# Optimization experiments

Measured on AMD Instinct MI355X. Metric: run time of the kernel, lower is better.

## Reference

```python
import jax, jax.numpy as jnp
import numpy as np

N, D, H, K = 131072, 512, 128, 3
NPOS, NNEG = 8192, 8192
KM_ITERS = 4
PROTO_SHIFT = 0.15
PROTO_LOGIT_SCALE = 0.2
TEMP = 2.5


def _sq_cdist(x, c):
    # squared euclidean distance, matches torch.cdist(...).pow(2)
    d = jnp.sum(x * x, -1, keepdims=True) + jnp.sum(c * c, -1)[None, :] - 2.0 * (x @ c.T)
    return jnp.maximum(d, 0.0)


def _kmeans(x, k, iters):
    # torch.linspace(0, n-1, steps=k).long() init, fixed iteration count
    n = x.shape[0]
    idx = jnp.linspace(0.0, n - 1, k).astype(jnp.int32)
    centers = x[idx]
    for _ in range(iters):
        assign = jnp.argmin(_sq_cdist(x, centers), axis=1)
        sums = jax.ops.segment_sum(x, assign, num_segments=k)
        counts = jax.ops.segment_sum(jnp.ones((n,), x.dtype), assign, num_segments=k)[:, None]
        # empty cluster keeps old center (mask.any() branch in torch)
        centers = jnp.where(counts > 0, sums / jnp.maximum(counts, 1.0), centers)
    return centers


def setup_inputs() -> dict:
    key = jax.random.key(0)
    ks = jax.random.split(key, 10)
    s = 1.0 / np.sqrt(D).astype(np.float32)
    return {
        "z_cls": jax.random.normal(ks[0], (N, D), jnp.float32),
        "z_proto": jax.random.normal(ks[1], (N, D), jnp.float32),
        "pos_ctx": jax.random.normal(ks[2], (D,), jnp.float32),
        "neg_ctx": jax.random.normal(ks[3], (D,), jnp.float32),
        "W1": jax.random.normal(ks[4], (H, D), jnp.float32) * s,
        "b1": jnp.zeros((H,), jnp.float32),
        "W2": jax.random.normal(ks[5], (1, H), jnp.float32) * (1.0 / np.sqrt(H).astype(np.float32)),
        "b2": jnp.zeros((1,), jnp.float32),
        "Wp": jax.random.normal(ks[6], (D, D), jnp.float32) * s,
        "bp": jnp.zeros((D,), jnp.float32),
        "Wn": jax.random.normal(ks[7], (D, D), jnp.float32) * s,
        "bn": jnp.zeros((D,), jnp.float32),
        "pos_idx": jax.random.randint(ks[8], (NPOS,), 0, N),
        "neg_idx": jax.random.randint(ks[9], (NNEG,), 0, N),
    }


def reference(z_cls, z_proto, pos_ctx, neg_ctx, W1, b1, W2, b2, Wp, bp, Wn, bn, pos_idx, neg_idx):
    # _build_prototypes (pos_idx/neg_idx nonempty path)
    pos_proto = _kmeans(z_proto[pos_idx], K, KM_ITERS)          # [K, D]
    neg_proto = jnp.mean(z_proto[neg_idx], axis=0)              # [D]
    # _calibrate (ema not initialized -> no EMA blend)
    pos_proto = pos_proto + PROTO_SHIFT * (pos_ctx @ Wp.T + bp)[None, :]
    neg_proto = neg_proto + PROTO_SHIFT * (neg_ctx @ Wn.T + bn)
    # distances
    d_pos_all = _sq_cdist(z_proto, pos_proto)                   # [N, K]
    d_pos = jnp.min(d_pos_all, axis=1)
    pos_assign = jnp.argmin(d_pos_all, axis=1)
    d_neg = jnp.mean((z_proto - neg_proto[None, :]) ** 2, axis=1)
    proto_logit = (d_neg - d_pos) / np.sqrt(D).astype(np.float32)
    # cls head (eval mode: dropout is identity)
    h = jax.nn.relu(z_cls @ W1.T + b1)
    cls_logit = (h @ W2.T + b2)[:, 0]
    logits = (cls_logit + PROTO_LOGIT_SCALE * proto_logit) / TEMP
    prob = jax.nn.sigmoid(logits)
    return (logits, prob, PROTO_LOGIT_SCALE * proto_logit, pos_assign, d_pos_all, pos_proto, neg_proto)
```

## Files before the change

### kernel.cpp

```cpp
#include <hip/hip_runtime.h>
#include <hip/hip_bf16.h>

#define NPTS 131072
#define DIM  512
#define HID  128
#define KCL  3
#define NPOSI 8192
#define NNEGI 8192

typedef __attribute__((ext_vector_type(8))) short bf16x8;
typedef __attribute__((ext_vector_type(4))) float f32x4;

#define ASG __attribute__((address_space(1)))
#define ASL __attribute__((address_space(3)))

enum {
  WS_SHIFT_POS = 0,
  WS_SHIFT_NEG = 512,
  WS_NEGSUM    = 1024,
  WS_NEGPART   = 1536,
  WS_SUMS      = 132608,
  WS_PPROTO    = 138764,
  WS_PN        = 140812,
  WS_W1FRAG    = 140816,
};
#define SUMS_STRIDE 1539

__device__ __forceinline__ short f2bf(float x) {
  __hip_bfloat16 h = __float2bfloat16(x);
  return *reinterpret_cast<short*>(&h);
}

__global__ __launch_bounds__(256, 1) void k_prep(const float* __restrict__ W1,
                                                 const float* __restrict__ Wp, const float* __restrict__ bp,
                                                 const float* __restrict__ Wn, const float* __restrict__ bn,
                                                 const float* __restrict__ pos_ctx, const float* __restrict__ neg_ctx,
                                                 const float* __restrict__ zp, const int* __restrict__ neg_idx,
                                                 float* __restrict__ ws) {
  int bid = blockIdx.x, t = threadIdx.x;
  if (bid < 32) {
    int fid = bid * 256 + t;
    int kc = fid >> 9;
    int n  = (fid >> 6) & 7;
    int l  = fid & 63;
    int row = n * 16 + (l & 15);
    int col = kc * 32 + (l >> 4) * 8;
    const float* src = W1 + (size_t)row * DIM + col;
    float4 v0 = *(const float4*)(src);
    float4 v1 = *(const float4*)(src + 4);
    bf16x8 f;
    f[0] = f2bf(v0.x); f[1] = f2bf(v0.y); f[2] = f2bf(v0.z); f[3] = f2bf(v0.w);
    f[4] = f2bf(v1.x); f[5] = f2bf(v1.y); f[6] = f2bf(v1.z); f[7] = f2bf(v1.w);
    ((bf16x8*)(ws + WS_W1FRAG))[fid] = f;
  } else if (bid < 64) {
    int b = bid - 32;
    int mat = b >> 4;
    const float* W    = mat ? Wn : Wp;
    const float* bias = mat ? bn : bp;
    const float* ctx  = mat ? neg_ctx : pos_ctx;
    float* outp = ws + (mat ? WS_SHIFT_NEG : WS_SHIFT_POS);
    int row = (b & 15) * 32 + (t >> 3);
    int sub = t & 7;
    const float* wr = W + row * DIM + sub * 64;
    const float* cr = ctx + sub * 64;
    float s = 0.f;
#pragma unroll
    for (int j = 0; j < 64; j += 4) {
      float4 w4 = *(const float4*)(wr + j);
      float4 c4 = *(const float4*)(cr + j);
      s += w4.x * c4.x + w4.y * c4.y + w4.z * c4.z + w4.w * c4.w;
    }
    s += __shfl_xor(s, 1);
    s += __shfl_xor(s, 2);
    s += __shfl_xor(s, 4);
    if (sub == 0) outp[row] = 0.15f * (s + bias[row]);
  } else if (bid < 320) {
    int jb = bid - 64;
    int c0 = t * 2;
    float a0 = 0.f, a1 = 0.f;
    int base = jb * 32;
#pragma unroll 8
    for (int jj = 0; jj < 32; ++jj) {
      int row = neg_idx[base + jj];
      float2 v = *(const float2*)(zp + (size_t)row * DIM + c0);
      a0 += v.x; a1 += v.y;
    }
    ws[WS_NEGPART + jb * DIM + c0]     = a0;
    ws[WS_NEGPART + jb * DIM + c0 + 1] = a1;
  } else {
    for (int idx = t; idx < 4 * SUMS_STRIDE; idx += 256) ws[WS_SUMS + idx] = 0.f;
  }
}

template <int IT>
__global__ __launch_bounds__(256, 1) void k_km(const float* __restrict__ zp,
                                               const int* __restrict__ pos_idx,
                                               float* __restrict__ ws) {
  int bid = blockIdx.x, t = threadIdx.x;
  if (IT == 0 && bid == 512) {
    int c0 = t * 2;
    float a0 = 0.f, a1 = 0.f;
#pragma unroll 8
    for (int j = 0; j < 256; ++j) {
      float2 v = *(const float2*)(ws + WS_NEGPART + j * DIM + c0);
      a0 += v.x; a1 += v.y;
    }
    ws[WS_NEGSUM + c0]     = a0;
    ws[WS_NEGSUM + c0 + 1] = a1;
    return;
  }
  __shared__ float cc[KCL * DIM];
  __shared__ float cn[KCL];
  __shared__ float lsum[KCL * DIM];
  __shared__ float lcnt[KCL];
  int w = t >> 6, l = t & 63;

  for (int idx = t; idx < KCL * DIM; idx += 256) lsum[idx] = 0.f;
  if (t < KCL) lcnt[t] = 0.f;

  for (int idx = t; idx < KCL * DIM; idx += 256) {
    int k = idx >> 9;
    int sel = (k == 0) ? 0 : ((k == 1) ? 4095 : 8191);
    float v = zp[(size_t)pos_idx[sel] * DIM + (idx & 511)];
#pragma unroll
    for (int j = 0; j < IT; ++j) {
      float cntv = ws[WS_SUMS + j * SUMS_STRIDE + 3 * DIM + k];
      float sv   = ws[WS_SUMS + j * SUMS_STRIDE + idx];
      v = (cntv > 0.f) ? sv / cntv : v;
    }
    cc[idx] = v;
  }
  __syncthreads();
  if (w < KCL) {
    float s = 0.f;
#pragma unroll
    for (int m = 0; m < 8; ++m) { float v = cc[w * DIM + l + m * 64]; s += v * v; }
#pragma unroll
    for (int m = 1; m < 64; m <<= 1) s += __shfl_xor(s, m);
    if (l == 0) cn[w] = s;
  }
  __syncthreads();

  float ck0[8], ck1[8], ck2[8];
#pragma unroll
  for (int j = 0; j < 8; ++j) {
    ck0[j] = cc[0 * DIM + l * 8 + j];
    ck1[j] = cc[1 * DIM + l * 8 + j];
    ck2[j] = cc[2 * DIM + l * 8 + j];
  }
  float cn0 = cn[0], cn1 = cn[1], cn2 = cn[2];
  float acc0[8] = {0,0,0,0,0,0,0,0}, acc1[8] = {0,0,0,0,0,0,0,0}, acc2[8] = {0,0,0,0,0,0,0,0};
  float cnt0 = 0.f, cnt1 = 0.f, cnt2 = 0.f;

  int wid = bid * 4 + w;
#pragma unroll 4
  for (int p = wid; p < NPOSI; p += 2048) {
    int row = pos_idx[p];
    const float* xr = zp + (size_t)row * DIM + l * 8;
    float4 x0 = *(const float4*)(xr);
    float4 x1 = *(const float4*)(xr + 4);
    float x[8] = {x0.x, x0.y, x0.z, x0.w, x1.x, x1.y, x1.z, x1.w};
    float d0 = 0.f, d1 = 0.f, d2 = 0.f;
#pragma unroll
    for (int j = 0; j < 8; ++j) { d0 += x[j] * ck0[j]; d1 += x[j] * ck1[j]; d2 += x[j] * ck2[j]; }
#pragma unroll
    for (int m = 1; m < 64; m <<= 1) {
      d0 += __shfl_xor(d0, m); d1 += __shfl_xor(d1, m); d2 += __shfl_xor(d2, m);
    }
    float t0 = cn0 - 2.f * d0, t1 = cn1 - 2.f * d1, t2 = cn2 - 2.f * d2;
    int a = 0; float best = t0;
    if (t1 < best) { best = t1; a = 1; }
    if (t2 < best) { best = t2; a = 2; }
    if (a == 0)      { cnt0 += 1.f;
#pragma unroll
      for (int j = 0; j < 8; ++j) acc0[j] += x[j]; }
    else if (a == 1) { cnt1 += 1.f;
#pragma unroll
      for (int j = 0; j < 8; ++j) acc1[j] += x[j]; }
    else             { cnt2 += 1.f;
#pragma unroll
      for (int j = 0; j < 8; ++j) acc2[j] += x[j]; }
  }
#pragma unroll
  for (int j = 0; j < 8; ++j) {
    atomicAdd(&lsum[0 * DIM + l * 8 + j], acc0[j]);
    atomicAdd(&lsum[1 * DIM + l * 8 + j], acc1[j]);
    atomicAdd(&lsum[2 * DIM + l * 8 + j], acc2[j]);
  }
  if (l == 0) {
    atomicAdd(&lcnt[0], cnt0); atomicAdd(&lcnt[1], cnt1); atomicAdd(&lcnt[2], cnt2);
  }
  __syncthreads();
  for (int idx = t; idx < KCL * DIM; idx += 256) atomicAdd(&ws[WS_SUMS + IT * SUMS_STRIDE + idx], lsum[idx]);
  if (t < KCL) atomicAdd(&ws[WS_SUMS + IT * SUMS_STRIDE + 3 * DIM + t], lcnt[t]);
}

__global__ __launch_bounds__(256) void k_fin(const float* __restrict__ zp,
                                             const int* __restrict__ pos_idx,
                                             float* __restrict__ ws, float* __restrict__ out) {
  __shared__ __align__(16) float pp[4 * DIM];
  int t = threadIdx.x, w = t >> 6, l = t & 63;
  for (int idx = t; idx < KCL * DIM; idx += 256) {
    int k = idx >> 9, d = idx & 511;
    int sel = (k == 0) ? 0 : ((k == 1) ? 4095 : 8191);
    float v = zp[(size_t)pos_idx[sel] * DIM + d];
#pragma unroll
    for (int j = 0; j < 4; ++j) {
      float cntv = ws[WS_SUMS + j * SUMS_STRIDE + 3 * DIM + k];
      float sv   = ws[WS_SUMS + j * SUMS_STRIDE + idx];
      v = (cntv > 0.f) ? sv / cntv : v;
    }
    pp[idx] = v + ws[WS_SHIFT_POS + d];
  }
  for (int d = t; d < DIM; d += 256)
    pp[3 * DIM + d] = ws[WS_NEGSUM + d] * (1.f / NNEGI) + ws[WS_SHIFT_NEG + d];
  __syncthreads();
  {
    float s = 0.f;
#pragma unroll
    for (int m = 0; m < 8; ++m) { float v = pp[w * DIM + l + m * 64]; s += v * v; }
#pragma unroll
    for (int m = 1; m < 64; m <<= 1) s += __shfl_xor(s, m);
    if (l == 0) ws[WS_PN + w] = s;
  }
  for (int idx = t; idx < 4 * DIM; idx += 256) {
    ws[WS_PPROTO + idx] = pp[idx];
    out[7 * NPTS + idx] = pp[idx];
  }
}

__global__ __launch_bounds__(256, 2) void k_fused(const float* __restrict__ zc,
                                                  const float* __restrict__ zp,
                                                  const float* __restrict__ b1,
                                                  const float* __restrict__ W2,
                                                  const float* __restrict__ b2,
                                                  const float* __restrict__ ws,
                                                  float* __restrict__ out) {
  __shared__ __align__(16) float Ast[2][16 * DIM];
  __shared__ __align__(16) float pp[4 * DIM];
  __shared__ float pns[4];
  __shared__ float clsv[32];

  int t = threadIdx.x, w = t >> 6, l = t & 63;
  int pr = w >> 1, hw = w & 1;
  int i0 = blockIdx.x * 32;
  int pairRow0 = i0 + pr * 16;

  if (t < 32) clsv[t] = 0.f;

  {
    const float* gsrc = zc + (size_t)(pairRow0 + hw * 8) * DIM;
    float* ldsb = &Ast[pr][0];
#pragma unroll
    for (int i = 0; i < 16; ++i) {
      int rloc = hw * 8 + (i >> 1);
      int c = ((i & 1) * 256) + ((l * 4) ^ ((rloc & 7) << 2));
      const float* src = gsrc + (size_t)(i >> 1) * DIM + c;
      float* dst = ldsb + rloc * DIM + (i & 1) * 256;
      __builtin_amdgcn_global_load_lds((const ASG void*)src, (ASL void*)dst, 16, 0, 0);
    }
  }

  for (int idx = t; idx < 4 * DIM; idx += 256) pp[idx] = ws[WS_PPROTO + idx];
  if (t < 4) pns[t] = ws[WS_PN + t];
  int col_l = l & 15;
  float b1c[4], w2c[4];
#pragma unroll
  for (int nn = 0; nn < 4; ++nn) {
    int col = (hw * 4 + nn) * 16 + col_l;
    b1c[nn] = b1[col];
    w2c[nn] = W2[col];
  }
  float b2v = b2[0];
  __syncthreads();

  {
    const bf16x8* w1f = (const bf16x8*)(ws + WS_W1FRAG);
    const float* pl = &Ast[pr][0];
    int sub = l >> 4, row = l & 15;
    int swz = (row & 7) << 2;
    int abase = row * DIM;
    f32x4 acc[4];
#pragma unroll
    for (int nn = 0; nn < 4; ++nn) acc[nn] = (f32x4){0.f, 0.f, 0.f, 0.f};
    bf16x8 B2[3][4];
#pragma unroll
    for (int pf = 0; pf < 3; ++pf)
#pragma unroll
      for (int nn = 0; nn < 4; ++nn)
        B2[pf][nn] = w1f[pf * 512 + (hw * 4 + nn) * 64 + l];

#pragma unroll
    for (int kc = 0; kc < 16; ++kc) {
      int g = kc * 32 + sub * 8;
      float4 a0 = *(const float4*)&pl[abase + (g ^ swz)];
      float4 a1 = *(const float4*)&pl[abase + ((g + 4) ^ swz)];
      if (kc + 3 < 16) {
#pragma unroll
        for (int nn = 0; nn < 4; ++nn)
          B2[kc % 3][nn] = w1f[(kc + 3) * 512 + (hw * 4 + nn) * 64 + l];
      }
      bf16x8 af;
      af[0] = f2bf(a0.x); af[1] = f2bf(a0.y); af[2] = f2bf(a0.z); af[3] = f2bf(a0.w);
      af[4] = f2bf(a1.x); af[5] = f2bf(a1.y); af[6] = f2bf(a1.z); af[7] = f2bf(a1.w);
#pragma unroll
      for (int nn = 0; nn < 4; ++nn)
        acc[nn] = __builtin_amdgcn_mfma_f32_16x16x32_bf16(af, B2[kc % 3][nn], acc[nn], 0, 0, 0);
    }
    float prt[4] = {0.f, 0.f, 0.f, 0.f};
#pragma unroll
    for (int nn = 0; nn < 4; ++nn) {
#pragma unroll
      for (int r = 0; r < 4; ++r) {
        float h = acc[nn][r] + b1c[nn];
        h = h > 0.f ? h : 0.f;
        prt[r] += h * w2c[nn];
      }
    }
#pragma unroll
    for (int m = 1; m < 16; m <<= 1) {
#pragma unroll
      for (int r = 0; r < 4; ++r) prt[r] += __shfl_xor(prt[r], m);
    }
    if (col_l == 0) {
      float add = hw ? 0.f : b2v;
#pragma unroll
      for (int r = 0; r < 4; ++r)
        atomicAdd(&clsv[pr * 16 + sub * 4 + r], prt[r] + add);
    }
  }
  __syncthreads();

  {
    const float* gsrc = zp + (size_t)(pairRow0 + hw * 8) * DIM;
    float* ldsb = &Ast[pr][0];
#pragma unroll
    for (int i = 0; i < 16; ++i) {
      int rloc = hw * 8 + (i >> 1);
      int c = ((i & 1) * 256) + ((l * 4) ^ ((rloc & 7) << 2));
      const float* src = gsrc + (size_t)(i >> 1) * DIM + c;
      float* dst = ldsb + rloc * DIM + (i & 1) * 256;
      __builtin_amdgcn_global_load_lds((const ASG void*)src, (ASL void*)dst, 16, 0, 0);
    }
  }
  __syncthreads();

  {
    int s = l & 7, r8 = l >> 3;
    const float* xl = &Ast[w >> 1][0];
    int rloc = (w & 1) * 8 + r8;
    int swz = (rloc & 7) << 2;
    int xbase = rloc * DIM;
    float d0 = 0.f, d1 = 0.f, d2 = 0.f, dn = 0.f, sx = 0.f;
#pragma unroll
    for (int j = 0; j < 16; ++j) {
      int c = j * 32 + s * 4;
      float4 x  = *(const float4*)&xl[xbase + (c ^ swz)];
      float4 c0 = *(const float4*)&pp[0 * DIM + c];
      float4 c1 = *(const float4*)&pp[1 * DIM + c];
      float4 c2 = *(const float4*)&pp[2 * DIM + c];
      float4 c3 = *(const float4*)&pp[3 * DIM + c];
      d0 += x.x * c0.x + x.y * c0.y + x.z * c0.z + x.w * c0.w;
      d1 += x.x * c1.x + x.y * c1.y + x.z * c1.z + x.w * c1.w;
      d2 += x.x * c2.x + x.y * c2.y + x.z * c2.z + x.w * c2.w;
      dn += x.x * c3.x + x.y * c3.y + x.z * c3.z + x.w * c3.w;
      sx += x.x * x.x  + x.y * x.y  + x.z * x.z  + x.w * x.w;
    }
#pragma unroll
    for (int m = 1; m < 8; m <<= 1) {
      d0 += __shfl_xor(d0, m);
      d1 += __shfl_xor(d1, m);
      d2 += __shfl_xor(d2, m);
      dn += __shfl_xor(dn, m);
      sx += __shfl_xor(sx, m);
    }
    if (s == 0) {
      int i = i0 + w * 8 + r8;
      float e0 = sx + pns[0] - 2.f * d0; e0 = fmaxf(e0, 0.f);
      float e1 = sx + pns[1] - 2.f * d1; e1 = fmaxf(e1, 0.f);
      float e2 = sx + pns[2] - 2.f * d2; e2 = fmaxf(e2, 0.f);
      float dpos = e0; int a = 0;
      if (e1 < dpos) { dpos = e1; a = 1; }
      if (e2 < dpos) { dpos = e2; a = 2; }
      float dneg = (sx + pns[3] - 2.f * dn) * (1.f / DIM);
      float plog = (dneg - dpos) * 0.04419417382415922f;
      float o2 = 0.2f * plog;
      float lg = (clsv[w * 8 + r8] + o2) * 0.4f;
      float prob = 1.f / (1.f + expf(-lg));
      out[i]            = lg;
      out[NPTS + i]     = prob;
      out[2 * NPTS + i] = o2;
      out[3 * NPTS + i] = (float)a;
      out[4 * NPTS + 3 * i]     = e0;
      out[4 * NPTS + 3 * i + 1] = e1;
      out[4 * NPTS + 3 * i + 2] = e2;
    }
  }
}

extern "C" void kernel_launch(void* const* d_in, const int* in_sizes, int n_in,
                              void* d_out, int out_size, void* d_ws, size_t ws_size,
                              hipStream_t stream) {
  const float* z_cls   = (const float*)d_in[0];
  const float* z_proto = (const float*)d_in[1];
  const float* pos_ctx = (const float*)d_in[2];
  const float* neg_ctx = (const float*)d_in[3];
  const float* W1      = (const float*)d_in[4];
  const float* b1      = (const float*)d_in[5];
  const float* W2      = (const float*)d_in[6];
  const float* b2      = (const float*)d_in[7];
  const float* Wp      = (const float*)d_in[8];
  const float* bp      = (const float*)d_in[9];
  const float* Wn      = (const float*)d_in[10];
  const float* bn      = (const float*)d_in[11];
  const int* pos_idx   = (const int*)d_in[12];
  const int* neg_idx   = (const int*)d_in[13];
  float* out           = (float*)d_out;
  float* ws            = (float*)d_ws;

  k_prep<<<321, 256, 0, stream>>>(W1, Wp, bp, Wn, bn, pos_ctx, neg_ctx, z_proto, neg_idx, ws);
  k_km<0><<<513, 256, 0, stream>>>(z_proto, pos_idx, ws);
  k_km<1><<<512, 256, 0, stream>>>(z_proto, pos_idx, ws);
  k_km<2><<<512, 256, 0, stream>>>(z_proto, pos_idx, ws);
  k_km<3><<<512, 256, 0, stream>>>(z_proto, pos_idx, ws);
  k_fin<<<1, 256, 0, stream>>>(z_proto, pos_idx, ws, out);
  k_fused<<<NPTS / 32, 256, 0, stream>>>(z_cls, z_proto, b1, W2, b2, ws, out);
}
```

Measured before the change: 274.5 us.

## Warp-specialize fused kernel to load z_cls and z_proto concurrently

The fused kernel moves to 512-thread blocks of 16 rows. Both the z_cls and z_proto tiles are issued to LDS up front. Warps 0-3 run the bf16 MFMA classifier head while warps 4-7 compute the prototype distances, replacing the old sequential load, compute, load, compute phases, with one barrier before the final output. Block indices are remapped in groups of 8 for XCD locality, and the k-means kernels use half as many blocks with a matching loop stride. The aim is to hide memory latency by keeping both streams in flight, at the cost of fewer MFMA columns per warp and higher LDS use per block.

```diff
diff --git a/kernel.cpp b/kernel.cpp
--- a/kernel.cpp
+++ b/kernel.cpp
@@ -93,11 +93,11 @@
 }
 
 template <int IT>
-__global__ __launch_bounds__(256, 1) void k_km(const float* __restrict__ zp,
-                                               const int* __restrict__ pos_idx,
-                                               float* __restrict__ ws) {
+__global__ __launch_bounds__(256) void k_km(const float* __restrict__ zp,
+                                            const int* __restrict__ pos_idx,
+                                            float* __restrict__ ws) {
   int bid = blockIdx.x, t = threadIdx.x;
-  if (IT == 0 && bid == 512) {
+  if (IT == 0 && bid == 256) {
     int c0 = t * 2;
     float a0 = 0.f, a1 = 0.f;
 #pragma unroll 8
@@ -153,8 +153,8 @@
   float cnt0 = 0.f, cnt1 = 0.f, cnt2 = 0.f;
 
   int wid = bid * 4 + w;
-#pragma unroll 4
-  for (int p = wid; p < NPOSI; p += 2048) {
+#pragma unroll 2
+  for (int p = wid; p < NPOSI; p += 1024) {
     int row = pos_idx[p];
     const float* xr = zp + (size_t)row * DIM + l * 8;
     float4 x0 = *(const float4*)(xr);
@@ -229,87 +229,92 @@
   }
 }
 
-__global__ __launch_bounds__(256, 2) void k_fused(const float* __restrict__ zc,
-                                                  const float* __restrict__ zp,
-                                                  const float* __restrict__ b1,
-                                                  const float* __restrict__ W2,
-                                                  const float* __restrict__ b2,
-                                                  const float* __restrict__ ws,
-                                                  float* __restrict__ out) {
-  __shared__ __align__(16) float Ast[2][16 * DIM];
+__global__ __launch_bounds__(512) void k_fused(const float* __restrict__ zc,
+                                               const float* __restrict__ zp,
+                                               const float* __restrict__ b1,
+                                               const float* __restrict__ W2,
+                                               const float* __restrict__ b2,
+                                               const float* __restrict__ ws,
+                                               float* __restrict__ out) {
+  __shared__ __align__(16) float Azc[16 * DIM];
+  __shared__ __align__(16) float Azp[16 * DIM];
   __shared__ __align__(16) float pp[4 * DIM];
   __shared__ float pns[4];
-  __shared__ float clsv[32];
+  __shared__ float clsv[16];
 
   int t = threadIdx.x, w = t >> 6, l = t & 63;
-  int pr = w >> 1, hw = w & 1;
-  int i0 = blockIdx.x * 32;
-  int pairRow0 = i0 + pr * 16;
-
-  if (t < 32) clsv[t] = 0.f;
+  int bid = (blockIdx.x & 7) * 1024 + (blockIdx.x >> 3);
+  int i0 = bid * 16;
 
   {
-    const float* gsrc = zc + (size_t)(pairRow0 + hw * 8) * DIM;
-    float* ldsb = &Ast[pr][0];
-#pragma unroll
-    for (int i = 0; i < 16; ++i) {
-      int rloc = hw * 8 + (i >> 1);
-      int c = ((i & 1) * 256) + ((l * 4) ^ ((rloc & 7) << 2));
-      const float* src = gsrc + (size_t)(i >> 1) * DIM + c;
-      float* dst = ldsb + rloc * DIM + (i & 1) * 256;
-      __builtin_amdgcn_global_load_lds((const ASG void*)src, (ASL void*)dst, 16, 0, 0);
-    }
-  }
-
-  for (int idx = t; idx < 4 * DIM; idx += 256) pp[idx] = ws[WS_PPROTO + idx];
+    int cg = (w < 4);
+    int r0 = (cg ? w : (w - 4)) * 4;
+    const float* gsrc = (cg ? zc : zp) + (size_t)(i0 + r0) * DIM;
+    float* ldsb = cg ? Azc : Azp;
+#pragma unroll
+    for (int r = 0; r < 4; ++r) {
+      int rloc = r0 + r;
+      int swz = (rloc & 7) << 2;
+#pragma unroll
+      for (int seg = 0; seg < 2; ++seg) {
+        int c = seg * 256 + ((l * 4) ^ swz);
+        __builtin_amdgcn_global_load_lds((const ASG void*)(gsrc + (size_t)r * DIM + c),
+                                         (ASL void*)&ldsb[rloc * DIM + seg * 256], 16, 0, 0);
+      }
+    }
+  }
+
+  if (t < 512) ((float4*)pp)[t] = ((const float4*)(ws + WS_PPROTO))[t];
+  if (t < 16) clsv[t] = 0.f;
   if (t < 4) pns[t] = ws[WS_PN + t];
   int col_l = l & 15;
-  float b1c[4], w2c[4];
-#pragma unroll
-  for (int nn = 0; nn < 4; ++nn) {
-    int col = (hw * 4 + nn) * 16 + col_l;
-    b1c[nn] = b1[col];
-    w2c[nn] = W2[col];
-  }
-  float b2v = b2[0];
-  __syncthreads();
-
-  {
+  float b1c[2], w2c[2], b2v = b2[0];
+  if (w < 4) {
+#pragma unroll
+    for (int nn = 0; nn < 2; ++nn) {
+      int col = (w * 2 + nn) * 16 + col_l;
+      b1c[nn] = b1[col];
+      w2c[nn] = W2[col];
+    }
+  }
+  __syncthreads();
+
+  float rd0 = 0.f, rd1 = 0.f, rd2 = 0.f, rdn = 0.f, rsx = 0.f;
+  if (w < 4) {
     const bf16x8* w1f = (const bf16x8*)(ws + WS_W1FRAG);
-    const float* pl = &Ast[pr][0];
-    int sub = l >> 4, row = l & 15;
-    int swz = (row & 7) << 2;
-    int abase = row * DIM;
-    f32x4 acc[4];
-#pragma unroll
-    for (int nn = 0; nn < 4; ++nn) acc[nn] = (f32x4){0.f, 0.f, 0.f, 0.f};
-    bf16x8 B2[3][4];
+    int sub = l >> 4, arow = l & 15;
+    int swz = (arow & 7) << 2;
+    int abase = arow * DIM;
+    f32x4 acc[2];
+    acc[0] = (f32x4){0.f, 0.f, 0.f, 0.f};
+    acc[1] = (f32x4){0.f, 0.f, 0.f, 0.f};
+    bf16x8 B2[3][2];
 #pragma unroll
     for (int pf = 0; pf < 3; ++pf)
 #pragma unroll
-      for (int nn = 0; nn < 4; ++nn)
-        B2[pf][nn] = w1f[pf * 512 + (hw * 4 + nn) * 64 + l];
+      for (int nn = 0; nn < 2; ++nn)
+        B2[pf][nn] = w1f[pf * 512 + (w * 2 + nn) * 64 + l];
 
 #pragma unroll
     for (int kc = 0; kc < 16; ++kc) {
       int g = kc * 32 + sub * 8;
-      float4 a0 = *(const float4*)&pl[abase + (g ^ swz)];
-      float4 a1 = *(const float4*)&pl[abase + ((g + 4) ^ swz)];
+      float4 a0 = *(const float4*)&Azc[abase + (g ^ swz)];
+      float4 a1 = *(const float4*)&Azc[abase + ((g + 4) ^ swz)];
       if (kc + 3 < 16) {
 #pragma unroll
-        for (int nn = 0; nn < 4; ++nn)
-          B2[kc % 3][nn] = w1f[(kc + 3) * 512 + (hw * 4 + nn) * 64 + l];
+        for (int nn = 0; nn < 2; ++nn)
+          B2[kc % 3][nn] = w1f[(kc + 3) * 512 + (w * 2 + nn) * 64 + l];
       }
       bf16x8 af;
       af[0] = f2bf(a0.x); af[1] = f2bf(a0.y); af[2] = f2bf(a0.z); af[3] = f2bf(a0.w);
       af[4] = f2bf(a1.x); af[5] = f2bf(a1.y); af[6] = f2bf(a1.z); af[7] = f2bf(a1.w);
 #pragma unroll
-      for (int nn = 0; nn < 4; ++nn)
+      for (int nn = 0; nn < 2; ++nn)
         acc[nn] = __builtin_amdgcn_mfma_f32_16x16x32_bf16(af, B2[kc % 3][nn], acc[nn], 0, 0, 0);
     }
     float prt[4] = {0.f, 0.f, 0.f, 0.f};
 #pragma unroll
-    for (int nn = 0; nn < 4; ++nn) {
+    for (int nn = 0; nn < 2; ++nn) {
 #pragma unroll
       for (int r = 0; r < 4; ++r) {
         float h = acc[nn][r] + b1c[nn];
@@ -323,78 +328,62 @@
       for (int r = 0; r < 4; ++r) prt[r] += __shfl_xor(prt[r], m);
     }
     if (col_l == 0) {
-      float add = hw ? 0.f : b2v;
+      float add = (w == 0) ? b2v : 0.f;
 #pragma unroll
       for (int r = 0; r < 4; ++r)
-        atomicAdd(&clsv[pr * 16 + sub * 4 + r], prt[r] + add);
-    }
-  }
-  __syncthreads();
-
-  {
-    const float* gsrc = zp + (size_t)(pairRow0 + hw * 8) * DIM;
-    float* ldsb = &Ast[pr][0];
-#pragma unroll
-    for (int i = 0; i < 16; ++i) {
-      int rloc = hw * 8 + (i >> 1);
-      int c = ((i & 1) * 256) + ((l * 4) ^ ((rloc & 7) << 2));
-      const float* src = gsrc + (size_t)(i >> 1) * DIM + c;
-      float* dst = ldsb + rloc * DIM + (i & 1) * 256;
-      __builtin_amdgcn_global_load_lds((const ASG void*)src, (ASL void*)dst, 16, 0, 0);
-    }
-  }
-  __syncthreads();
-
-  {
-    int s = l & 7, r8 = l >> 3;
-    const float* xl = &Ast[w >> 1][0];
-    int rloc = (w & 1) * 8 + r8;
+        atomicAdd(&clsv[sub * 4 + r], prt[r] + add);
+    }
+  } else {
+    int s = l & 15, r4 = l >> 4;
+    int rloc = (w - 4) * 4 + r4;
     int swz = (rloc & 7) << 2;
     int xbase = rloc * DIM;
-    float d0 = 0.f, d1 = 0.f, d2 = 0.f, dn = 0.f, sx = 0.f;
-#pragma unroll
-    for (int j = 0; j < 16; ++j) {
-      int c = j * 32 + s * 4;
-      float4 x  = *(const float4*)&xl[xbase + (c ^ swz)];
+#pragma unroll
+    for (int j = 0; j < 8; ++j) {
+      int c = j * 64 + s * 4;
+      float4 x  = *(const float4*)&Azp[xbase + (c ^ swz)];
       float4 c0 = *(const float4*)&pp[0 * DIM + c];
       float4 c1 = *(const float4*)&pp[1 * DIM + c];
       float4 c2 = *(const float4*)&pp[2 * DIM + c];
       float4 c3 = *(const float4*)&pp[3 * DIM + c];
-      d0 += x.x * c0.x + x.y * c0.y + x.z * c0.z + x.w * c0.w;
-      d1 += x.x * c1.x + x.y * c1.y + x.z * c1.z + x.w * c1.w;
-      d2 += x.x * c2.x + x.y * c2.y + x.z * c2.z + x.w * c2.w;
-      dn += x.x * c3.x + x.y * c3.y + x.z * c3.z + x.w * c3.w;
-      sx += x.x * x.x  + x.y * x.y  + x.z * x.z  + x.w * x.w;
-    }
-#pragma unroll
-    for (int m = 1; m < 8; m <<= 1) {
-      d0 += __shfl_xor(d0, m);
-      d1 += __shfl_xor(d1, m);
-      d2 += __shfl_xor(d2, m);
-      dn += __shfl_xor(dn, m);
-      sx += __shfl_xor(sx, m);
-    }
-    if (s == 0) {
-      int i = i0 + w * 8 + r8;
-      float e0 = sx + pns[0] - 2.f * d0; e0 = fmaxf(e0, 0.f);
-      float e1 = sx + pns[1] - 2.f * d1; e1 = fmaxf(e1, 0.f);
-      float e2 = sx + pns[2] - 2.f * d2; e2 = fmaxf(e2, 0.f);
-      float dpos = e0; int a = 0;
-      if (e1 < dpos) { dpos = e1; a = 1; }
-      if (e2 < dpos) { dpos = e2; a = 2; }
-      float dneg = (sx + pns[3] - 2.f * dn) * (1.f / DIM);
-      float plog = (dneg - dpos) * 0.04419417382415922f;
-      float o2 = 0.2f * plog;
-      float lg = (clsv[w * 8 + r8] + o2) * 0.4f;
-      float prob = 1.f / (1.f + expf(-lg));
-      out[i]            = lg;
-      out[NPTS + i]     = prob;
-      out[2 * NPTS + i] = o2;
-      out[3 * NPTS + i] = (float)a;
-      out[4 * NPTS + 3 * i]     = e0;
-      out[4 * NPTS + 3 * i + 1] = e1;
-      out[4 * NPTS + 3 * i + 2] = e2;
-    }
+      rd0 += x.x * c0.x + x.y * c0.y + x.z * c0.z + x.w * c0.w;
+      rd1 += x.x * c1.x + x.y * c1.y + x.z * c1.z + x.w * c1.w;
+      rd2 += x.x * c2.x + x.y * c2.y + x.z * c2.z + x.w * c2.w;
+      rdn += x.x * c3.x + x.y * c3.y + x.z * c3.z + x.w * c3.w;
+      rsx += x.x * x.x  + x.y * x.y  + x.z * x.z  + x.w * x.w;
+    }
+#pragma unroll
+    for (int m = 1; m < 16; m <<= 1) {
+      rd0 += __shfl_xor(rd0, m);
+      rd1 += __shfl_xor(rd1, m);
+      rd2 += __shfl_xor(rd2, m);
+      rdn += __shfl_xor(rdn, m);
+      rsx += __shfl_xor(rsx, m);
+    }
+  }
+  __syncthreads();
+
+  if (w >= 4 && (l & 15) == 0) {
+    int rloc = (w - 4) * 4 + (l >> 4);
+    int i = i0 + rloc;
+    float e0 = rsx + pns[0] - 2.f * rd0; e0 = fmaxf(e0, 0.f);
+    float e1 = rsx + pns[1] - 2.f * rd1; e1 = fmaxf(e1, 0.f);
+    float e2 = rsx + pns[2] - 2.f * rd2; e2 = fmaxf(e2, 0.f);
+    float dpos = e0; int a = 0;
+    if (e1 < dpos) { dpos = e1; a = 1; }
+    if (e2 < dpos) { dpos = e2; a = 2; }
+    float dneg = (rsx + pns[3] - 2.f * rdn) * (1.f / DIM);
+    float plog = (dneg - dpos) * 0.04419417382415922f;
+    float o2 = 0.2f * plog;
+    float lg = (clsv[rloc] + o2) * 0.4f;
+    float prob = 1.f / (1.f + expf(-lg));
+    out[i]            = lg;
+    out[NPTS + i]     = prob;
+    out[2 * NPTS + i] = o2;
+    out[3 * NPTS + i] = (float)a;
+    out[4 * NPTS + 3 * i]     = e0;
+    out[4 * NPTS + 3 * i + 1] = e1;
+    out[4 * NPTS + 3 * i + 2] = e2;
   }
 }
 
@@ -419,10 +408,10 @@
   float* ws            = (float*)d_ws;
 
   k_prep<<<321, 256, 0, stream>>>(W1, Wp, bp, Wn, bn, pos_ctx, neg_ctx, z_proto, neg_idx, ws);
-  k_km<0><<<513, 256, 0, stream>>>(z_proto, pos_idx, ws);
-  k_km<1><<<512, 256, 0, stream>>>(z_proto, pos_idx, ws);
-  k_km<2><<<512, 256, 0, stream>>>(z_proto, pos_idx, ws);
-  k_km<3><<<512, 256, 0, stream>>>(z_proto, pos_idx, ws);
+  k_km<0><<<257, 256, 0, stream>>>(z_proto, pos_idx, ws);
+  k_km<1><<<256, 256, 0, stream>>>(z_proto, pos_idx, ws);
+  k_km<2><<<256, 256, 0, stream>>>(z_proto, pos_idx, ws);
+  k_km<3><<<256, 256, 0, stream>>>(z_proto, pos_idx, ws);
   k_fin<<<1, 256, 0, stream>>>(z_proto, pos_idx, ws, out);
-  k_fused<<<NPTS / 32, 256, 0, stream>>>(z_cls, z_proto, b1, W2, b2, ws, out);
-}
+  k_fused<<<NPTS / 16, 512, 0, stream>>>(z_cls, z_proto, b1, W2, b2, ws, out);
+}
```

Result: slower. 283.8 us (+3.4%).

## Merge prep, k-means iterations and finalize into one cooperative kernel

Applied to the files above, without the earlier changes.

Six small launches (prep, four k-means iterations, finalize) are replaced by one cooperative kernel of 257 blocks that uses grid-wide syncs between phases. The goal is to remove per-launch overhead and the idle gaps between tiny dependent kernels. The k-means grid shrinks from 512 to 256 blocks, so each wave now strides over twice as many points. Grid syncs add their own cost, and cooperative launch needs all blocks resident at once.

```diff
diff --git a/kernel.cpp b/kernel.cpp
--- a/kernel.cpp
+++ b/kernel.cpp
@@ -1,5 +1,8 @@
 #include <hip/hip_runtime.h>
 #include <hip/hip_bf16.h>
+#include <hip/hip_cooperative_groups.h>
+
+namespace cg = cooperative_groups;
 
 #define NPTS 131072
 #define DIM  512
@@ -31,20 +34,30 @@
   return *reinterpret_cast<short*>(&h);
 }
 
-__global__ __launch_bounds__(256, 1) void k_prep(const float* __restrict__ W1,
-                                                 const float* __restrict__ Wp, const float* __restrict__ bp,
-                                                 const float* __restrict__ Wn, const float* __restrict__ bn,
-                                                 const float* __restrict__ pos_ctx, const float* __restrict__ neg_ctx,
-                                                 const float* __restrict__ zp, const int* __restrict__ neg_idx,
-                                                 float* __restrict__ ws) {
+__global__ __launch_bounds__(256) void k_tail(const float* __restrict__ W1,
+                                              const float* __restrict__ Wp, const float* __restrict__ bp,
+                                              const float* __restrict__ Wn, const float* __restrict__ bn,
+                                              const float* __restrict__ pos_ctx, const float* __restrict__ neg_ctx,
+                                              const float* __restrict__ zp,
+                                              const int* __restrict__ neg_idx, const int* __restrict__ pos_idx,
+                                              float* __restrict__ ws, float* __restrict__ out) {
+  cg::grid_group grid = cg::this_grid();
   int bid = blockIdx.x, t = threadIdx.x;
+  int w = t >> 6, l = t & 63;
+
+  __shared__ float cc[KCL * DIM];
+  __shared__ float cn[KCL];
+  __shared__ float lsum[KCL * DIM];
+  __shared__ float lcnt[KCL];
+  __shared__ __align__(16) float pp[4 * DIM];
+
   if (bid < 32) {
     int fid = bid * 256 + t;
     int kc = fid >> 9;
     int n  = (fid >> 6) & 7;
-    int l  = fid & 63;
-    int row = n * 16 + (l & 15);
-    int col = kc * 32 + (l >> 4) * 8;
+    int ll = fid & 63;
+    int row = n * 16 + (ll & 15);
+    int col = kc * 32 + (ll >> 4) * 8;
     const float* src = W1 + (size_t)row * DIM + col;
     float4 v0 = *(const float4*)(src);
     float4 v1 = *(const float4*)(src + 4);
@@ -74,158 +87,147 @@
     s += __shfl_xor(s, 2);
     s += __shfl_xor(s, 4);
     if (sub == 0) outp[row] = 0.15f * (s + bias[row]);
-  } else if (bid < 320) {
-    int jb = bid - 64;
+  } else if (bid == 256) {
+    for (int idx = t; idx < 4 * SUMS_STRIDE; idx += 256) ws[WS_SUMS + idx] = 0.f;
+  }
+  if (bid < 256) {
     int c0 = t * 2;
     float a0 = 0.f, a1 = 0.f;
-    int base = jb * 32;
+    int base = bid * 32;
 #pragma unroll 8
     for (int jj = 0; jj < 32; ++jj) {
       int row = neg_idx[base + jj];
       float2 v = *(const float2*)(zp + (size_t)row * DIM + c0);
       a0 += v.x; a1 += v.y;
     }
-    ws[WS_NEGPART + jb * DIM + c0]     = a0;
-    ws[WS_NEGPART + jb * DIM + c0 + 1] = a1;
-  } else {
-    for (int idx = t; idx < 4 * SUMS_STRIDE; idx += 256) ws[WS_SUMS + idx] = 0.f;
-  }
-}
-
-template <int IT>
-__global__ __launch_bounds__(256, 1) void k_km(const float* __restrict__ zp,
-                                               const int* __restrict__ pos_idx,
-                                               float* __restrict__ ws) {
-  int bid = blockIdx.x, t = threadIdx.x;
-  if (IT == 0 && bid == 512) {
-    int c0 = t * 2;
-    float a0 = 0.f, a1 = 0.f;
+    ws[WS_NEGPART + bid * DIM + c0]     = a0;
+    ws[WS_NEGPART + bid * DIM + c0 + 1] = a1;
+  }
+  grid.sync();
+
+  for (int it = 0; it < 4; ++it) {
+    if (bid == 256) {
+      if (it == 0) {
+        int c0 = t * 2;
+        float a0 = 0.f, a1 = 0.f;
 #pragma unroll 8
-    for (int j = 0; j < 256; ++j) {
-      float2 v = *(const float2*)(ws + WS_NEGPART + j * DIM + c0);
-      a0 += v.x; a1 += v.y;
-    }
-    ws[WS_NEGSUM + c0]     = a0;
-    ws[WS_NEGSUM + c0 + 1] = a1;
-    return;
-  }
-  __shared__ float cc[KCL * DIM];
-  __shared__ float cn[KCL];
-  __shared__ float lsum[KCL * DIM];
-  __shared__ float lcnt[KCL];
-  int w = t >> 6, l = t & 63;
-
-  for (int idx = t; idx < KCL * DIM; idx += 256) lsum[idx] = 0.f;
-  if (t < KCL) lcnt[t] = 0.f;
-
-  for (int idx = t; idx < KCL * DIM; idx += 256) {
-    int k = idx >> 9;
-    int sel = (k == 0) ? 0 : ((k == 1) ? 4095 : 8191);
-    float v = zp[(size_t)pos_idx[sel] * DIM + (idx & 511)];
-#pragma unroll
-    for (int j = 0; j < IT; ++j) {
-      float cntv = ws[WS_SUMS + j * SUMS_STRIDE + 3 * DIM + k];
-      float sv   = ws[WS_SUMS + j * SUMS_STRIDE + idx];
-      v = (cntv > 0.f) ? sv / cntv : v;
-    }
-    cc[idx] = v;
-  }
-  __syncthreads();
-  if (w < KCL) {
-    float s = 0.f;
-#pragma unroll
-    for (int m = 0; m < 8; ++m) { float v = cc[w * DIM + l + m * 64]; s += v * v; }
-#pragma unroll
-    for (int m = 1; m < 64; m <<= 1) s += __shfl_xor(s, m);
-    if (l == 0) cn[w] = s;
-  }
-  __syncthreads();
-
-  float ck0[8], ck1[8], ck2[8];
-#pragma unroll
-  for (int j = 0; j < 8; ++j) {
-    ck0[j] = cc[0 * DIM + l * 8 + j];
-    ck1[j] = cc[1 * DIM + l * 8 + j];
-    ck2[j] = cc[2 * DIM + l * 8 + j];
-  }
-  float cn0 = cn[0], cn1 = cn[1], cn2 = cn[2];
-  float acc0[8] = {0,0,0,0,0,0,0,0}, acc1[8] = {0,0,0,0,0,0,0,0}, acc2[8] = {0,0,0,0,0,0,0,0};
-  float cnt0 = 0.f, cnt1 = 0.f, cnt2 = 0.f;
-
-  int wid = bid * 4 + w;
-#pragma unroll 4
-  for (int p = wid; p < NPOSI; p += 2048) {
-    int row = pos_idx[p];
-    const float* xr = zp + (size_t)row * DIM + l * 8;
-    float4 x0 = *(const float4*)(xr);
-    float4 x1 = *(const float4*)(xr + 4);
-    float x[8] = {x0.x, x0.y, x0.z, x0.w, x1.x, x1.y, x1.z, x1.w};
-    float d0 = 0.f, d1 = 0.f, d2 = 0.f;
-#pragma unroll
-    for (int j = 0; j < 8; ++j) { d0 += x[j] * ck0[j]; d1 += x[j] * ck1[j]; d2 += x[j] * ck2[j]; }
-#pragma unroll
-    for (int m = 1; m < 64; m <<= 1) {
-      d0 += __shfl_xor(d0, m); d1 += __shfl_xor(d1, m); d2 += __shfl_xor(d2, m);
-    }
-    float t0 = cn0 - 2.f * d0, t1 = cn1 - 2.f * d1, t2 = cn2 - 2.f * d2;
-    int a = 0; float best = t0;
-    if (t1 < best) { best = t1; a = 1; }
-    if (t2 < best) { best = t2; a = 2; }
-    if (a == 0)      { cnt0 += 1.f;
-#pragma unroll
-      for (int j = 0; j < 8; ++j) acc0[j] += x[j]; }
-    else if (a == 1) { cnt1 += 1.f;
-#pragma unroll
-      for (int j = 0; j < 8; ++j) acc1[j] += x[j]; }
-    else             { cnt2 += 1.f;
-#pragma unroll
-      for (int j = 0; j < 8; ++j) acc2[j] += x[j]; }
-  }
-#pragma unroll
-  for (int j = 0; j < 8; ++j) {
-    atomicAdd(&lsum[0 * DIM + l * 8 + j], acc0[j]);
-    atomicAdd(&lsum[1 * DIM + l * 8 + j], acc1[j]);
-    atomicAdd(&lsum[2 * DIM + l * 8 + j], acc2[j]);
-  }
-  if (l == 0) {
-    atomicAdd(&lcnt[0], cnt0); atomicAdd(&lcnt[1], cnt1); atomicAdd(&lcnt[2], cnt2);
-  }
-  __syncthreads();
-  for (int idx = t; idx < KCL * DIM; idx += 256) atomicAdd(&ws[WS_SUMS + IT * SUMS_STRIDE + idx], lsum[idx]);
-  if (t < KCL) atomicAdd(&ws[WS_SUMS + IT * SUMS_STRIDE + 3 * DIM + t], lcnt[t]);
-}
-
-__global__ __launch_bounds__(256) void k_fin(const float* __restrict__ zp,
-                                             const int* __restrict__ pos_idx,
-                                             float* __restrict__ ws, float* __restrict__ out) {
-  __shared__ __align__(16) float pp[4 * DIM];
-  int t = threadIdx.x, w = t >> 6, l = t & 63;
-  for (int idx = t; idx < KCL * DIM; idx += 256) {
-    int k = idx >> 9, d = idx & 511;
-    int sel = (k == 0) ? 0 : ((k == 1) ? 4095 : 8191);
-    float v = zp[(size_t)pos_idx[sel] * DIM + d];
-#pragma unroll
-    for (int j = 0; j < 4; ++j) {
-      float cntv = ws[WS_SUMS + j * SUMS_STRIDE + 3 * DIM + k];
-      float sv   = ws[WS_SUMS + j * SUMS_STRIDE + idx];
-      v = (cntv > 0.f) ? sv / cntv : v;
-    }
-    pp[idx] = v + ws[WS_SHIFT_POS + d];
-  }
-  for (int d = t; d < DIM; d += 256)
-    pp[3 * DIM + d] = ws[WS_NEGSUM + d] * (1.f / NNEGI) + ws[WS_SHIFT_NEG + d];
-  __syncthreads();
-  {
-    float s = 0.f;
-#pragma unroll
-    for (int m = 0; m < 8; ++m) { float v = pp[w * DIM + l + m * 64]; s += v * v; }
-#pragma unroll
-    for (int m = 1; m < 64; m <<= 1) s += __shfl_xor(s, m);
-    if (l == 0) ws[WS_PN + w] = s;
-  }
-  for (int idx = t; idx < 4 * DIM; idx += 256) {
-    ws[WS_PPROTO + idx] = pp[idx];
-    out[7 * NPTS + idx] = pp[idx];
+        for (int j = 0; j < 256; ++j) {
+          float2 v = *(const float2*)(ws + WS_NEGPART + j * DIM + c0);
+          a0 += v.x; a1 += v.y;
+        }
+        ws[WS_NEGSUM + c0]     = a0;
+        ws[WS_NEGSUM + c0 + 1] = a1;
+      }
+    } else {
+      for (int idx = t; idx < KCL * DIM; idx += 256) lsum[idx] = 0.f;
+      if (t < KCL) lcnt[t] = 0.f;
+
+      for (int idx = t; idx < KCL * DIM; idx += 256) {
+        int k = idx >> 9;
+        int sel = (k == 0) ? 0 : ((k == 1) ? 4095 : 8191);
+        float v = zp[(size_t)pos_idx[sel] * DIM + (idx & 511)];
+        for (int j = 0; j < it; ++j) {
+          float cntv = ws[WS_SUMS + j * SUMS_STRIDE + 3 * DIM + k];
+          float sv   = ws[WS_SUMS + j * SUMS_STRIDE + idx];
+          v = (cntv > 0.f) ? sv / cntv : v;
+        }
+        cc[idx] = v;
+      }
+      __syncthreads();
+      if (w < KCL) {
+        float s = 0.f;
+#pragma unroll
+        for (int m = 0; m < 8; ++m) { float v = cc[w * DIM + l + m * 64]; s += v * v; }
+#pragma unroll
+        for (int m = 1; m < 64; m <<= 1) s += __shfl_xor(s, m);
+        if (l == 0) cn[w] = s;
+      }
+      __syncthreads();
+
+      float ck0[8], ck1[8], ck2[8];
+#pragma unroll
+      for (int j = 0; j < 8; ++j) {
+        ck0[j] = cc[0 * DIM + l * 8 + j];
+        ck1[j] = cc[1 * DIM + l * 8 + j];
+        ck2[j] = cc[2 * DIM + l * 8 + j];
+      }
+      float cn0 = cn[0], cn1 = cn[1], cn2 = cn[2];
+      float acc0[8] = {0,0,0,0,0,0,0,0}, acc1[8] = {0,0,0,0,0,0,0,0}, acc2[8] = {0,0,0,0,0,0,0,0};
+      float cnt0 = 0.f, cnt1 = 0.f, cnt2 = 0.f;
+
+      int wid = bid * 4 + w;
+#pragma unroll 2
+      for (int p = wid; p < NPOSI; p += 1024) {
+        int row = pos_idx[p];
+        const float* xr = zp + (size_t)row * DIM + l * 8;
+        float4 x0 = *(const float4*)(xr);
+        float4 x1 = *(const float4*)(xr + 4);
+        float x[8] = {x0.x, x0.y, x0.z, x0.w, x1.x, x1.y, x1.z, x1.w};
+        float d0 = 0.f, d1 = 0.f, d2 = 0.f;
+#pragma unroll
+        for (int j = 0; j < 8; ++j) { d0 += x[j] * ck0[j]; d1 += x[j] * ck1[j]; d2 += x[j] * ck2[j]; }
+#pragma unroll
+        for (int m = 1; m < 64; m <<= 1) {
+          d0 += __shfl_xor(d0, m); d1 += __shfl_xor(d1, m); d2 += __shfl_xor(d2, m);
+        }
+        float t0 = cn0 - 2.f * d0, t1 = cn1 - 2.f * d1, t2 = cn2 - 2.f * d2;
+        int a = 0; float best = t0;
+        if (t1 < best) { best = t1; a = 1; }
+        if (t2 < best) { best = t2; a = 2; }
+        if (a == 0)      { cnt0 += 1.f;
+#pragma unroll
+          for (int j = 0; j < 8; ++j) acc0[j] += x[j]; }
+        else if (a == 1) { cnt1 += 1.f;
+#pragma unroll
+          for (int j = 0; j < 8; ++j) acc1[j] += x[j]; }
+        else             { cnt2 += 1.f;
+#pragma unroll
+          for (int j = 0; j < 8; ++j) acc2[j] += x[j]; }
+      }
+#pragma unroll
+      for (int j = 0; j < 8; ++j) {
+        atomicAdd(&lsum[0 * DIM + l * 8 + j], acc0[j]);
+        atomicAdd(&lsum[1 * DIM + l * 8 + j], acc1[j]);
+        atomicAdd(&lsum[2 * DIM + l * 8 + j], acc2[j]);
+      }
+      if (l == 0) {
+        atomicAdd(&lcnt[0], cnt0); atomicAdd(&lcnt[1], cnt1); atomicAdd(&lcnt[2], cnt2);
+      }
+      __syncthreads();
+      for (int idx = t; idx < KCL * DIM; idx += 256) atomicAdd(&ws[WS_SUMS + it * SUMS_STRIDE + idx], lsum[idx]);
+      if (t < KCL) atomicAdd(&ws[WS_SUMS + it * SUMS_STRIDE + 3 * DIM + t], lcnt[t]);
+    }
+    grid.sync();
+  }
+
+  if (bid == 0) {
+    for (int idx = t; idx < KCL * DIM; idx += 256) {
+      int k = idx >> 9, d = idx & 511;
+      int sel = (k == 0) ? 0 : ((k == 1) ? 4095 : 8191);
+      float v = zp[(size_t)pos_idx[sel] * DIM + d];
+#pragma unroll
+      for (int j = 0; j < 4; ++j) {
+        float cntv = ws[WS_SUMS + j * SUMS_STRIDE + 3 * DIM + k];
+        float sv   = ws[WS_SUMS + j * SUMS_STRIDE + idx];
+        v = (cntv > 0.f) ? sv / cntv : v;
+      }
+      pp[idx] = v + ws[WS_SHIFT_POS + d];
+    }
+    for (int d = t; d < DIM; d += 256)
+      pp[3 * DIM + d] = ws[WS_NEGSUM + d] * (1.f / NNEGI) + ws[WS_SHIFT_NEG + d];
+    __syncthreads();
+    {
+      float s = 0.f;
+#pragma unroll
+      for (int m = 0; m < 8; ++m) { float v = pp[w * DIM + l + m * 64]; s += v * v; }
+#pragma unroll
+      for (int m = 1; m < 64; m <<= 1) s += __shfl_xor(s, m);
+      if (l == 0) ws[WS_PN + w] = s;
+    }
+    for (int idx = t; idx < 4 * DIM; idx += 256) {
+      ws[WS_PPROTO + idx] = pp[idx];
+      out[7 * NPTS + idx] = pp[idx];
+    }
   }
 }
 
@@ -418,11 +420,11 @@
   float* out           = (float*)d_out;
   float* ws            = (float*)d_ws;
 
-  k_prep<<<321, 256, 0, stream>>>(W1, Wp, bp, Wn, bn, pos_ctx, neg_ctx, z_proto, neg_idx, ws);
-  k_km<0><<<513, 256, 0, stream>>>(z_proto, pos_idx, ws);
-  k_km<1><<<512, 256, 0, stream>>>(z_proto, pos_idx, ws);
-  k_km<2><<<512, 256, 0, stream>>>(z_proto, pos_idx, ws);
-  k_km<3><<<512, 256, 0, stream>>>(z_proto, pos_idx, ws);
-  k_fin<<<1, 256, 0, stream>>>(z_proto, pos_idx, ws, out);
+  void* args[] = {
+    (void*)&W1, (void*)&Wp, (void*)&bp, (void*)&Wn, (void*)&bn,
+    (void*)&pos_ctx, (void*)&neg_ctx, (void*)&z_proto,
+    (void*)&neg_idx, (void*)&pos_idx, (void*)&ws, (void*)&out
+  };
+  hipLaunchCooperativeKernel((void*)k_tail, dim3(257), dim3(256), args, 0, stream);
   k_fused<<<NPTS / 32, 256, 0, stream>>>(z_cls, z_proto, b1, W2, b2, ws, out);
 }
```

Result: slower. 368.0 us (+34.0%).
